# Kernel optimization log

Measured on AMD Instinct MI355X. Metric: run time of the kernel, lower is better.

The kernel has to match this reference:

```python
import jax, jax.numpy as jnp
import numpy as np

B, N, H, D, DEPTH = 16, 1024, 2, 128, 3
A = H * D  # atten_dim = 256
FFN = 1024
EPS = 1e-5


def layer_norm(x, g, b):
    mu = jnp.mean(x, axis=-1, keepdims=True)
    var = jnp.mean(jnp.square(x - mu), axis=-1, keepdims=True)
    return (x - mu) * jax.lax.rsqrt(var + EPS) * g + b


def setup_inputs() -> dict:
    key = jax.random.key(0)
    ks = jax.random.split(key, 16)
    s = lambda fan_in: 1.0 / np.sqrt(fan_in)
    inp = {
        "X": jax.random.normal(ks[0], (B, N, A), jnp.float32),
        # per-layer attention projections, stacked over depth
        "Wq": jax.random.normal(ks[1], (DEPTH, A, A), jnp.float32) * s(A),
        "bq": jnp.zeros((DEPTH, A), jnp.float32),
        "Wk": jax.random.normal(ks[2], (DEPTH, A, A), jnp.float32) * s(A),
        "bk": jnp.zeros((DEPTH, A), jnp.float32),
        "Wv": jax.random.normal(ks[3], (DEPTH, A, A), jnp.float32) * s(A),
        "bv": jnp.zeros((DEPTH, A), jnp.float32),
        # per-layer FFN (roll_out): Linear(A,1024)+ReLU, Linear(1024,A)+ReLU
        "W1": jax.random.normal(ks[4], (DEPTH, A, FFN), jnp.float32) * s(A),
        "b1": jnp.zeros((DEPTH, FFN), jnp.float32),
        "W2": jax.random.normal(ks[5], (DEPTH, FFN, A), jnp.float32) * s(FFN),
        "b2": jnp.zeros((DEPTH, A), jnp.float32),
        # single shared LayerNorm (the torch module reuses one instance)
        "ln_g": jnp.ones((A,), jnp.float32),
        "ln_b": jnp.zeros((A,), jnp.float32),
        # Conv1d(A, A, kernel_size=1) == per-position linear over channels
        "Wc": jax.random.normal(ks[6], (A, A), jnp.float32) * s(A),
        "bc": jnp.zeros((A,), jnp.float32),
        # final Linear(A, A) on pooled features
        "We": jax.random.normal(ks[7], (A, A), jnp.float32) * s(A),
        "be": jnp.zeros((A,), jnp.float32),
    }
    return inp


def reference(X, Wq, bq, Wk, bk, Wv, bv, W1, b1, W2, b2, ln_g, ln_b, Wc, bc, We, be):
    inv_sqrt_d = 1.0 / np.sqrt(D)
    step = X  # [B, N, A]
    for i in range(DEPTH):
        q = (step @ Wq[i] + bq[i]).reshape(B, N, H, D).transpose(0, 2, 1, 3)
        k = (step @ Wk[i] + bk[i]).reshape(B, N, H, D).transpose(0, 2, 1, 3)
        v = (step @ Wv[i] + bv[i]).reshape(B, N, H, D).transpose(0, 2, 1, 3)
        scores = jnp.einsum('bhqd,bhkd->bhqk', q, k) * inv_sqrt_d
        probs = jax.nn.softmax(scores, axis=-1)
        attn = jnp.einsum('bhqk,bhkd->bhqd', probs, v)
        attn = attn.transpose(0, 2, 1, 3).reshape(B, N, A)
        roll = jax.nn.relu(jax.nn.relu(attn @ W1[i] + b1[i]) @ W2[i] + b2[i])
        step = layer_norm(roll + step, ln_g, ln_b)
    # Conv1d(kernel=1) + ReLU over channels, per position
    entity_encodings = jax.nn.relu(step @ Wc + bc)  # [B, N, A]
    pooled = jnp.mean(entity_encodings, axis=1)      # [B, A]
    encoded_entities = jax.nn.relu(pooled @ We + be)  # [B, A]
    return encoded_entities
```

## Files before the change

kernel.cpp:

```cpp
#include <hip/hip_runtime.h>
#include <hip/hip_bf16.h>
#include <cstddef>

#define B_   16
#define N_   1024
#define H_   2
#define D_   128
#define A_   256
#define FFN_ 1024
#define M_   (B_ * N_)
#define EPS_ 1e-5f
#define SPLIT 4
#define KT   32
#define TPC  (N_ / SPLIT / KT)
#define QKV_E ((size_t)B_ * H_ * N_ * D_)

typedef short  short8  __attribute__((ext_vector_type(8)));
typedef float  f32x16  __attribute__((ext_vector_type(16)));
typedef unsigned int uint;
typedef unsigned short ushort;

#define MFMA32(a, b, c) __builtin_amdgcn_mfma_f32_32x32x16_bf16(a, b, c, 0, 0, 0)

__device__ __forceinline__ uint f2b1(float x) {
    uint u = __float_as_uint(x);
    return (u + 0x7fffu + ((u >> 16) & 1u)) >> 16;
}
__device__ __forceinline__ uint f2b2(float lo, float hi) {
    return f2b1(lo) | (f2b1(hi) << 16);
}
__device__ __forceinline__ float b2f(ushort u) {
    return __uint_as_float(((uint)u) << 16);
}

__global__ __launch_bounds__(256) void f32_to_bf16_kernel(
    const float* __restrict__ in, ushort* __restrict__ out)
{
    const size_t i = ((size_t)blockIdx.x * 256 + threadIdx.x) * 8;
    float4 a = *(const float4*)(in + i);
    float4 b = *(const float4*)(in + i + 4);
    uint4 w = { f2b2(a.x, a.y), f2b2(a.z, a.w), f2b2(b.x, b.y), f2b2(b.z, b.w) };
    *(uint4*)(out + i) = w;
}

__global__ __launch_bounds__(256) void prep_kernel(
    const float* __restrict__ Wq, const float* __restrict__ Wk,
    const float* __restrict__ Wv, const float* __restrict__ W1,
    const float* __restrict__ W2, const float* __restrict__ Wc,
    ushort* __restrict__ wqkv_t, ushort* __restrict__ w1_t,
    ushort* __restrict__ w2_t, ushort* __restrict__ wc_t)
{
    const int z = blockIdx.z;
    const float* W; ushort* out; int K, N, n0, k0;
    if (z < 9) {
        const int layer = z / 3, sec = z % 3;
        W = (sec == 0 ? Wq : sec == 1 ? Wk : Wv) + (size_t)layer * A_ * A_;
        out = wqkv_t + (size_t)layer * 3 * A_ * A_ + (size_t)sec * A_ * A_;
        K = A_; N = A_;
        n0 = blockIdx.x * 32; k0 = blockIdx.y * 32;
    } else if (z < 12) {
        const int layer = z - 9;
        W = W1 + (size_t)layer * A_ * FFN_; out = w1_t + (size_t)layer * A_ * FFN_;
        K = A_; N = FFN_;
        n0 = blockIdx.x * 32; k0 = blockIdx.y * 32;
    } else if (z < 15) {
        const int layer = z - 12;
        W = W2 + (size_t)layer * FFN_ * A_; out = w2_t + (size_t)layer * FFN_ * A_;
        K = FFN_; N = A_;
        k0 = blockIdx.x * 32; n0 = blockIdx.y * 32;
    } else {
        W = Wc; out = wc_t; K = A_; N = A_;
        n0 = blockIdx.x * 32; k0 = blockIdx.y * 32;
    }
    if (n0 >= N || k0 >= K) return;

    __shared__ float tile[32][33];
    const int tc = threadIdx.x & 31, tr = threadIdx.x >> 5;
#pragma unroll
    for (int it = 0; it < 4; ++it) {
        int r = it * 8 + tr;
        tile[r][tc] = W[(size_t)(k0 + r) * N + n0 + tc];
    }
    __syncthreads();
#pragma unroll
    for (int it = 0; it < 4; ++it) {
        int r = it * 8 + tr;
        out[(size_t)(n0 + r) * K + k0 + tc] = (ushort)f2b1(tile[tc][r]);
    }
}

template <int MR>
__global__ __launch_bounds__(256) void gemm_mfma(
    const ushort* __restrict__ Asrc, const ushort* __restrict__ Wt,
    const float* __restrict__ bias, const float* __restrict__ biasK,
    const float* __restrict__ biasV, void* __restrict__ outp,
    int K, int ldc, int mode)
{
    constexpr int BM = MR * 64;
    __shared__ ushort sA[BM * 72];
    __shared__ ushort sB[128 * 72];

    const int tid = threadIdx.x;
    const int wid = tid >> 6, lane = tid & 63;
    const int c = lane & 31, g = lane >> 5;
    const int wr = wid >> 1, wc = wid & 1;
    const int m0 = blockIdx.x * BM;
    const int n0 = blockIdx.y * 128;

    f32x16 acc[MR][2] = {};

    for (int k0 = 0; k0 < K; k0 += 64) {
        __syncthreads();
#pragma unroll
        for (int it = 0; it < BM / 32; ++it) {
            int idx = it * 256 + tid, r = idx >> 3, cc = (idx & 7) * 8;
            *(uint4*)&sA[r * 72 + cc] =
                *(const uint4*)(Asrc + (size_t)(m0 + r) * K + k0 + cc);
        }
#pragma unroll
        for (int it = 0; it < 4; ++it) {
            int idx = it * 256 + tid, r = idx >> 3, cc = (idx & 7) * 8;
            *(uint4*)&sB[r * 72 + cc] =
                *(const uint4*)(Wt + (size_t)(n0 + r) * K + k0 + cc);
        }
        __syncthreads();
#pragma unroll
        for (int ks = 0; ks < 4; ++ks) {
            const int ko = ks * 16 + 8 * g;
            short8 b0 = *(const short8*)&sB[(wc * 64 + c) * 72 + ko];
            short8 b1 = *(const short8*)&sB[(wc * 64 + 32 + c) * 72 + ko];
#pragma unroll
            for (int mr = 0; mr < MR; ++mr) {
                short8 a = *(const short8*)&sA[((wr * MR + mr) * 32 + c) * 72 + ko];
                acc[mr][0] = MFMA32(a, b0, acc[mr][0]);
                acc[mr][1] = MFMA32(a, b1, acc[mr][1]);
            }
        }
    }

    const int sec = n0 >> 8;
    const float* bp = bias;
    int nw = n0;
    if (mode == 5) {
        bp = (sec == 0 ? bias : sec == 1 ? biasK : biasV);
        nw = n0 & 255;
    }
    const float bz[2] = { bp[nw + wc * 64 + c], bp[nw + wc * 64 + 32 + c] };

    float colsum[2] = { 0.f, 0.f };

#pragma unroll
    for (int mr = 0; mr < MR; ++mr) {
#pragma unroll
        for (int ct = 0; ct < 2; ++ct) {
            const int colbase = n0 + wc * 64 + ct * 32 + c;
#pragma unroll
            for (int rg = 0; rg < 4; ++rg) {
                const int row = m0 + (wr * MR + mr) * 32 + 8 * rg + 4 * g;
                float v0 = acc[mr][ct][4 * rg + 0] + bz[ct];
                float v1 = acc[mr][ct][4 * rg + 1] + bz[ct];
                float v2 = acc[mr][ct][4 * rg + 2] + bz[ct];
                float v3 = acc[mr][ct][4 * rg + 3] + bz[ct];
                if (mode == 1 || mode == 2 || mode == 6) {
                    v0 = fmaxf(v0, 0.f); v1 = fmaxf(v1, 0.f);
                    v2 = fmaxf(v2, 0.f); v3 = fmaxf(v3, 0.f);
                }
                if (mode == 1) {
                    float* o = (float*)outp;
                    o[(size_t)(row + 0) * ldc + colbase] = v0;
                    o[(size_t)(row + 1) * ldc + colbase] = v1;
                    o[(size_t)(row + 2) * ldc + colbase] = v2;
                    o[(size_t)(row + 3) * ldc + colbase] = v3;
                } else if (mode == 2) {
                    ushort* o = (ushort*)outp;
                    o[(size_t)(row + 0) * ldc + colbase] = (ushort)f2b1(v0);
                    o[(size_t)(row + 1) * ldc + colbase] = (ushort)f2b1(v1);
                    o[(size_t)(row + 2) * ldc + colbase] = (ushort)f2b1(v2);
                    o[(size_t)(row + 3) * ldc + colbase] = (ushort)f2b1(v3);
                } else if (mode == 6) {
                    colsum[ct] += v0 + v1 + v2 + v3;
                } else {
                    const int cw = colbase & 255;
                    const int hh = cw >> 7, dd = cw & (D_ - 1);
                    if (sec < 2) {
                        ushort* o = (ushort*)outp + (size_t)sec * QKV_E;
#pragma unroll
                        for (int r2 = 0; r2 < 4; ++r2) {
                            int rw = row + r2;
                            int bb = rw >> 10, np = rw & (N_ - 1);
                            float vv = (r2 == 0 ? v0 : r2 == 1 ? v1 : r2 == 2 ? v2 : v3);
                            size_t off = (((size_t)(bb * H_ + hh) * 32 + (np >> 5)) * 16
                                          + (dd >> 3)) * 256
                                         + (np & 31) * 8 + (dd & 7);
                            o[off] = (ushort)f2b1(vv);
                        }
                    } else {
                        ushort* o = (ushort*)outp + 2 * QKV_E;
                        const int bb = row >> 10, np = row & (N_ - 1);
                        size_t off = ((((size_t)(bb * H_ + hh) * 32 + (np >> 5)) * 4
                                       + (dd >> 5)) * 4 + ((np & 31) >> 3)) * 256
                                     + (dd & 31) * 8 + (np & 7);
                        uint2 w = { f2b2(v0, v1), f2b2(v2, v3) };
                        *(uint2*)(o + off) = w;
                    }
                }
            }
        }
    }

    if (mode == 6) {
        float* part = (float*)outp;
        const int b = m0 >> 10;
#pragma unroll
        for (int ct = 0; ct < 2; ++ct) {
            float cs = colsum[ct] + __shfl_xor(colsum[ct], 32, 64);
            if (g == 0)
                atomicAdd(&part[(size_t)b * A_ + n0 + wc * 64 + ct * 32 + c], cs);
        }
    }
}

#define OPITCH 132

__global__ __launch_bounds__(128, 3) void attn_kernel(
    const ushort* __restrict__ qg, const ushort* __restrict__ kg,
    const ushort* __restrict__ vtg, ushort* __restrict__ po,
    float* __restrict__ pm, float* __restrict__ pl)
{
    __shared__ ushort sO[64 * OPITCH];

    const int tid = threadIdx.x;
    const int w = tid >> 6, lane = tid & 63;
    const int c = lane & 31, g = lane >> 5;

    const int flat = blockIdx.x;
    const int xcd  = flat & 7;
    const int ii   = flat >> 3;
    const int pair = xcd * 16 + (ii & 15);
    const int qt   = ii >> 4;
    const int bh   = pair & 31;
    const int z    = pair >> 5;

    const int q0 = qt * 64 + w * 32;
    const float scale2 = 0.08838834764831845f * 1.44269504f;
    const float THR = 11.5f;
    const int lo8 = c * 8;

    short8 qf[8];
    const ushort* qt_ = qg + ((size_t)bh * 32 + (q0 >> 5)) * 4096;
#pragma unroll
    for (int ks = 0; ks < 8; ++ks)
        qf[ks] = *(const short8*)(qt_ + (2 * ks + g) * 256 + lo8);

    f32x16 oacc[4] = {};
    float m = -1e30f, l = 0.f;

    for (int t = 0; t < TPC; ++t) {
        const size_t tb = ((size_t)bh * 32 + z * 8 + t) * 4096;
        const ushort* kt_ = kg + tb;
        const ushort* vt_ = vtg + tb;

        f32x16 sacc = {};
        __builtin_amdgcn_s_setprio(1);
#pragma unroll
        for (int ks = 0; ks < 8; ++ks) {
            short8 a = *(const short8*)(kt_ + (2 * ks + g) * 256 + lo8);
            sacc = MFMA32(a, qf[ks], sacc);
        }
        __builtin_amdgcn_s_setprio(0);

        const ushort* vb = vt_ + g * 256 + lo8;
        short8 vfA0 = *(const short8*)(vb + 0 * 1024);
        short8 vfA1 = *(const short8*)(vb + 1 * 1024);
        short8 vfA2 = *(const short8*)(vb + 2 * 1024);
        short8 vfA3 = *(const short8*)(vb + 3 * 1024);
        short8 vfB0 = *(const short8*)(vb + 0 * 1024 + 512);
        short8 vfB1 = *(const short8*)(vb + 1 * 1024 + 512);
        short8 vfB2 = *(const short8*)(vb + 2 * 1024 + 512);
        short8 vfB3 = *(const short8*)(vb + 3 * 1024 + 512);
        __builtin_amdgcn_sched_barrier(0);

        float p[16];
        float tmax = -1e30f;
#pragma unroll
        for (int r = 0; r < 16; ++r) {
            float s = sacc[r] * scale2;
            p[r] = s;
            tmax = fmaxf(tmax, s);
        }
        tmax = fmaxf(tmax, __shfl_xor(tmax, 32, 64));
        if (!__all(tmax - m <= THR)) {
            const float mnew = fmaxf(m, tmax);
            const float corr = exp2f(m - mnew);
#pragma unroll
            for (int dt = 0; dt < 4; ++dt)
#pragma unroll
                for (int r = 0; r < 16; ++r) oacc[dt][r] *= corr;
            l *= corr;
            m = mnew;
        }
        float tsum = 0.f;
#pragma unroll
        for (int r = 0; r < 16; ++r) {
            p[r] = exp2f(p[r] - m);
            tsum += p[r];
        }
        tsum += __shfl_xor(tsum, 32, 64);
        l += tsum;

        uint pk[8];
#pragma unroll
        for (int pp = 0; pp < 8; ++pp)
            pk[pp] = f2b2(p[2 * pp], p[2 * pp + 1]);

        uint v0 = g ? pk[0] : pk[2];
        uint v1 = g ? pk[1] : pk[3];
        uint v2 = g ? pk[4] : pk[6];
        uint v3 = g ? pk[5] : pk[7];
        uint r0 = (uint)__shfl_xor((int)v0, 32, 64);
        uint r1 = (uint)__shfl_xor((int)v1, 32, 64);
        uint r2 = (uint)__shfl_xor((int)v2, 32, 64);
        uint r3 = (uint)__shfl_xor((int)v3, 32, 64);

        __builtin_amdgcn_s_setprio(1);
#pragma unroll
        for (int kb = 0; kb < 2; ++kb) {
            union { uint u[4]; short8 s; } pf;
            if (kb == 0) {
                pf.u[0] = g ? r0 : pk[0];
                pf.u[1] = g ? r1 : pk[1];
                pf.u[2] = g ? pk[2] : r0;
                pf.u[3] = g ? pk[3] : r1;
            } else {
                pf.u[0] = g ? r2 : pk[4];
                pf.u[1] = g ? r3 : pk[5];
                pf.u[2] = g ? pk[6] : r2;
                pf.u[3] = g ? pk[7] : r3;
            }
            oacc[0] = MFMA32(kb ? vfB0 : vfA0, pf.s, oacc[0]);
            oacc[1] = MFMA32(kb ? vfB1 : vfA1, pf.s, oacc[1]);
            oacc[2] = MFMA32(kb ? vfB2 : vfA2, pf.s, oacc[2]);
            oacc[3] = MFMA32(kb ? vfB3 : vfA3, pf.s, oacc[3]);
        }
        __builtin_amdgcn_s_setprio(0);
    }

    if (lane < 32) {
        pm[(size_t)(z * 32 + bh) * N_ + q0 + c] = m;
        pl[(size_t)(z * 32 + bh) * N_ + q0 + c] = l;
    }
    {
        const int qrl = w * 32 + c;
#pragma unroll
        for (int dt = 0; dt < 4; ++dt)
#pragma unroll
            for (int rg = 0; rg < 4; ++rg) {
                int d = dt * 32 + 8 * rg + 4 * g;
                uint2 pv = { f2b2(oacc[dt][4 * rg + 0], oacc[dt][4 * rg + 1]),
                             f2b2(oacc[dt][4 * rg + 2], oacc[dt][4 * rg + 3]) };
                *(uint2*)&sO[qrl * OPITCH + d] = pv;
            }
    }
    __syncthreads();
    {
        const size_t pbase = ((size_t)(z * 32 + bh) * N_ + qt * 64) * D_;
#pragma unroll
        for (int it = 0; it < 16; ++it) {
            int idx = it * 128 + tid;
            int r = idx >> 5, dgr = (idx & 31) * 4;
            uint2 v = *(const uint2*)&sO[r * OPITCH + dgr];
            *(uint2*)(po + pbase + (size_t)r * D_ + dgr) = v;
        }
    }
}

__global__ __launch_bounds__(256) void combine_kernel(
    const ushort* __restrict__ po, const float* __restrict__ pm,
    const float* __restrict__ pl, ushort* __restrict__ out)
{
    const int idx = blockIdx.x * 256 + threadIdx.x;
    const int row = idx >> 4, d0 = (idx & 15) * 8;
    const int R = B_ * H_ * N_;

    float ms[SPLIT];
    float M = -1e30f;
#pragma unroll
    for (int s = 0; s < SPLIT; ++s) {
        ms[s] = pm[(size_t)s * R + row];
        M = fmaxf(M, ms[s]);
    }
    float L = 0.f;
    float acc[8] = {};
#pragma unroll
    for (int s = 0; s < SPLIT; ++s) {
        float wgt = exp2f(ms[s] - M);
        L += pl[(size_t)s * R + row] * wgt;
        uint4 pv = *(const uint4*)(po + ((size_t)s * R + row) * D_ + d0);
        const ushort* pu = (const ushort*)&pv;
#pragma unroll
        for (int j = 0; j < 8; ++j) acc[j] += b2f(pu[j]) * wgt;
    }
    const float inv = 1.f / L;
    uint4 w;
    w.x = f2b2(acc[0] * inv, acc[1] * inv);
    w.y = f2b2(acc[2] * inv, acc[3] * inv);
    w.z = f2b2(acc[4] * inv, acc[5] * inv);
    w.w = f2b2(acc[6] * inv, acc[7] * inv);
    const int bh = row >> 10, n = row & (N_ - 1);
    const int bb = bh >> 1, hh = bh & 1;
    *(uint4*)(out + ((size_t)(bb * N_ + n)) * A_ + hh * D_ + d0) = w;
}

__global__ __launch_bounds__(256) void add_ln_kernel(
    const ushort* __restrict__ roll, const float* __restrict__ prev,
    const float* __restrict__ g, const float* __restrict__ bta,
    float* __restrict__ out, ushort* __restrict__ outb)
{
    const int row = blockIdx.x * 4 + (threadIdx.x >> 6);
    const int lane = threadIdx.x & 63, c4 = lane * 4;
    const size_t base = (size_t)row * A_ + c4;

    uint2 rb = *(const uint2*)(roll + base);
    float4 pv = *(const float4*)(prev + base);
    float v0 = b2f((ushort)(rb.x & 0xffff)) + pv.x;
    float v1 = b2f((ushort)(rb.x >> 16))    + pv.y;
    float v2 = b2f((ushort)(rb.y & 0xffff)) + pv.z;
    float v3 = b2f((ushort)(rb.y >> 16))    + pv.w;

    float s  = v0 + v1 + v2 + v3;
    float s2 = v0 * v0 + v1 * v1 + v2 * v2 + v3 * v3;
#pragma unroll
    for (int o = 32; o > 0; o >>= 1) {
        s  += __shfl_xor(s, o, 64);
        s2 += __shfl_xor(s2, o, 64);
    }
    const float mu = s * (1.f / A_);
    const float rs = rsqrtf(s2 * (1.f / A_) - mu * mu + EPS_);

    float4 gv = *(const float4*)(g + c4);
    float4 bv = *(const float4*)(bta + c4);
    float y0 = (v0 - mu) * rs * gv.x + bv.x;
    float y1 = (v1 - mu) * rs * gv.y + bv.y;
    float y2 = (v2 - mu) * rs * gv.z + bv.z;
    float y3 = (v3 - mu) * rs * gv.w + bv.w;

    float4 yo = { y0, y1, y2, y3 };
    *(float4*)(out + base) = yo;
    uint2 yb = { f2b2(y0, y1), f2b2(y2, y3) };
    *(uint2*)(outb + base) = yb;
}

__global__ __launch_bounds__(256) void final_kernel(
    const float* __restrict__ part, const float* __restrict__ We,
    const float* __restrict__ be, float* __restrict__ out)
{
    __shared__ float sp[A_];
    const int b = blockIdx.x, tid = threadIdx.x;
    sp[tid] = part[(size_t)b * A_ + tid] * (1.0f / N_);
    __syncthreads();
    float acc = be[tid];
    for (int kk = 0; kk < A_; ++kk) acc += sp[kk] * We[(size_t)kk * A_ + tid];
    out[b * A_ + tid] = fmaxf(acc, 0.f);
}

extern "C" void kernel_launch(void* const* d_in, const int* in_sizes, int n_in,
                              void* d_out, int out_size, void* d_ws, size_t ws_size,
                              hipStream_t stream)
{
    const float* X    = (const float*)d_in[0];
    const float* Wq   = (const float*)d_in[1];
    const float* bq   = (const float*)d_in[2];
    const float* Wk   = (const float*)d_in[3];
    const float* bk   = (const float*)d_in[4];
    const float* Wv   = (const float*)d_in[5];
    const float* bv   = (const float*)d_in[6];
    const float* W1   = (const float*)d_in[7];
    const float* b1   = (const float*)d_in[8];
    const float* W2   = (const float*)d_in[9];
    const float* b2   = (const float*)d_in[10];
    const float* ln_g = (const float*)d_in[11];
    const float* ln_b = (const float*)d_in[12];
    const float* Wc   = (const float*)d_in[13];
    const float* bc   = (const float*)d_in[14];
    const float* We   = (const float*)d_in[15];
    const float* be   = (const float*)d_in[16];

    char* base = (char*)d_ws;
    ushort* qb     = (ushort*)base;  base += QKV_E * 2;
                             base += QKV_E * 2;
                             base += QKV_E * 2;
    ushort* hbuf   = (ushort*)base;  base += (size_t)M_ * FFN_ * 2;
    ushort* rollb  = (ushort*)base;  base += (size_t)M_ * A_ * 2;
    float*  step   = (float*)base;   base += (size_t)M_ * A_ * 4;
    ushort* stepb  = (ushort*)base;  base += (size_t)M_ * A_ * 2;
    ushort* wqkv_t = (ushort*)base;  base += (size_t)3 * 3 * A_ * A_ * 2;
    ushort* w1_t   = (ushort*)base;  base += (size_t)3 * A_ * FFN_ * 2;
    ushort* w2_t   = (ushort*)base;  base += (size_t)3 * FFN_ * A_ * 2;
    ushort* wc_t   = (ushort*)base;  base += (size_t)A_ * A_ * 2;
    float*  part   = (float*)base;   base += (size_t)B_ * A_ * 4;
    float*  pm     = (float*)base;   base += (size_t)SPLIT * B_ * H_ * N_ * 4;
    float*  pl     = (float*)base;   base += (size_t)SPLIT * B_ * H_ * N_ * 4;
    ushort* kbuf   = qb + QKV_E;
    ushort* vtbuf  = qb + 2 * QKV_E;
    ushort* po     = hbuf;
    ushort* attnb  = qb;

    prep_kernel<<<dim3(32, 8, 16), 256, 0, stream>>>(
        Wq, Wk, Wv, W1, W2, Wc, wqkv_t, w1_t, w2_t, wc_t);
    f32_to_bf16_kernel<<<(M_ * A_) / (256 * 8), 256, 0, stream>>>(X, stepb);

    const float* cur = X;
    for (int i = 0; i < 3; ++i) {
        gemm_mfma<2><<<dim3(M_/128, 6), 256, 0, stream>>>(
            stepb, wqkv_t + (size_t)i * 3 * A_ * A_,
            bq + i * A_, bk + i * A_, bv + i * A_, qb, A_, 0, 5);

        attn_kernel<<<16 * SPLIT * B_ * H_, 128, 0, stream>>>(
            qb, kbuf, vtbuf, po, pm, pl);
        combine_kernel<<<(B_*H_*N_*D_)/(256*8), 256, 0, stream>>>(po, pm, pl, attnb);

        gemm_mfma<2><<<dim3(M_/128, FFN_/128), 256, 0, stream>>>(
            attnb, w1_t + (size_t)i * A_ * FFN_, b1 + i * FFN_, nullptr, nullptr,
            hbuf, A_, FFN_, 2);
        gemm_mfma<1><<<dim3(M_/64, A_/128), 256, 0, stream>>>(
            hbuf, w2_t + (size_t)i * FFN_ * A_, b2 + i * A_, nullptr, nullptr,
            rollb, FFN_, A_, 2);

        add_ln_kernel<<<M_/4, 256, 0, stream>>>(rollb, cur, ln_g, ln_b, step, stepb);
        cur = step;
    }

    hipMemsetAsync(part, 0, (size_t)B_ * A_ * 4, stream);
    gemm_mfma<1><<<dim3(M_/64, A_/128), 256, 0, stream>>>(
        stepb, wc_t, bc, nullptr, nullptr, part, A_, 0, 6);
    final_kernel<<<B_, 256, 0, stream>>>(part, We, be, (float*)d_out);
}
```

Measured before the change: 385.1 us.

## Prefetch next K tile in attention and keep residual stream in bf16

The attention kernel now loads the next K tile into registers while the current tile's QK MFMAs run, and issues the V loads before the score MFMAs. Launch bounds are lowered from 3 to 2 blocks per SM to make room for the extra registers. The add+LayerNorm kernel no longer reads and writes a float32 residual. It reads the bf16 step buffer as the residual and updates it in place, which cuts memory traffic but lowers the precision of the residual path, including the first layer's use of X.

```diff
diff --git a/kernel.cpp b/kernel.cpp
--- a/kernel.cpp
+++ b/kernel.cpp
@@ -222,7 +222,7 @@
 
 #define OPITCH 132
 
-__global__ __launch_bounds__(128, 3) void attn_kernel(
+__global__ __launch_bounds__(128, 2) void attn_kernel(
     const ushort* __restrict__ qg, const ushort* __restrict__ kg,
     const ushort* __restrict__ vtg, ushort* __restrict__ po,
     float* __restrict__ pm, float* __restrict__ pl)
@@ -255,21 +255,21 @@
     f32x16 oacc[4] = {};
     float m = -1e30f, l = 0.f;
 
+    const size_t chunk0 = ((size_t)bh * 32 + z * 8) * 4096;
+    const ushort* kb0 = kg + chunk0 + g * 256 + lo8;
+    short8 kf0 = *(const short8*)(kb0 + 0 * 512);
+    short8 kf1 = *(const short8*)(kb0 + 1 * 512);
+    short8 kf2 = *(const short8*)(kb0 + 2 * 512);
+    short8 kf3 = *(const short8*)(kb0 + 3 * 512);
+    short8 kf4 = *(const short8*)(kb0 + 4 * 512);
+    short8 kf5 = *(const short8*)(kb0 + 5 * 512);
+    short8 kf6 = *(const short8*)(kb0 + 6 * 512);
+    short8 kf7 = *(const short8*)(kb0 + 7 * 512);
+
     for (int t = 0; t < TPC; ++t) {
-        const size_t tb = ((size_t)bh * 32 + z * 8 + t) * 4096;
-        const ushort* kt_ = kg + tb;
-        const ushort* vt_ = vtg + tb;
-
-        f32x16 sacc = {};
-        __builtin_amdgcn_s_setprio(1);
-#pragma unroll
-        for (int ks = 0; ks < 8; ++ks) {
-            short8 a = *(const short8*)(kt_ + (2 * ks + g) * 256 + lo8);
-            sacc = MFMA32(a, qf[ks], sacc);
-        }
-        __builtin_amdgcn_s_setprio(0);
-
-        const ushort* vb = vt_ + g * 256 + lo8;
+        const size_t tb = chunk0 + (size_t)t * 4096;
+
+        const ushort* vb = vtg + tb + g * 256 + lo8;
         short8 vfA0 = *(const short8*)(vb + 0 * 1024);
         short8 vfA1 = *(const short8*)(vb + 1 * 1024);
         short8 vfA2 = *(const short8*)(vb + 2 * 1024);
@@ -278,6 +278,31 @@
         short8 vfB1 = *(const short8*)(vb + 1 * 1024 + 512);
         short8 vfB2 = *(const short8*)(vb + 2 * 1024 + 512);
         short8 vfB3 = *(const short8*)(vb + 3 * 1024 + 512);
+        __builtin_amdgcn_sched_barrier(0);
+
+        f32x16 sacc = {};
+        __builtin_amdgcn_s_setprio(1);
+        sacc = MFMA32(kf0, qf[0], sacc);
+        sacc = MFMA32(kf1, qf[1], sacc);
+        sacc = MFMA32(kf2, qf[2], sacc);
+        sacc = MFMA32(kf3, qf[3], sacc);
+        sacc = MFMA32(kf4, qf[4], sacc);
+        sacc = MFMA32(kf5, qf[5], sacc);
+        sacc = MFMA32(kf6, qf[6], sacc);
+        sacc = MFMA32(kf7, qf[7], sacc);
+        __builtin_amdgcn_s_setprio(0);
+
+        if (t + 1 < TPC) {
+            const ushort* kb2 = kg + tb + 4096 + g * 256 + lo8;
+            kf0 = *(const short8*)(kb2 + 0 * 512);
+            kf1 = *(const short8*)(kb2 + 1 * 512);
+            kf2 = *(const short8*)(kb2 + 2 * 512);
+            kf3 = *(const short8*)(kb2 + 3 * 512);
+            kf4 = *(const short8*)(kb2 + 4 * 512);
+            kf5 = *(const short8*)(kb2 + 5 * 512);
+            kf6 = *(const short8*)(kb2 + 6 * 512);
+            kf7 = *(const short8*)(kb2 + 7 * 512);
+        }
         __builtin_amdgcn_sched_barrier(0);
 
         float p[16];
@@ -412,20 +437,19 @@
 }
 
 __global__ __launch_bounds__(256) void add_ln_kernel(
-    const ushort* __restrict__ roll, const float* __restrict__ prev,
-    const float* __restrict__ g, const float* __restrict__ bta,
-    float* __restrict__ out, ushort* __restrict__ outb)
+    const ushort* __restrict__ roll, ushort* __restrict__ stepb,
+    const float* __restrict__ g, const float* __restrict__ bta)
 {
     const int row = blockIdx.x * 4 + (threadIdx.x >> 6);
     const int lane = threadIdx.x & 63, c4 = lane * 4;
     const size_t base = (size_t)row * A_ + c4;
 
     uint2 rb = *(const uint2*)(roll + base);
-    float4 pv = *(const float4*)(prev + base);
-    float v0 = b2f((ushort)(rb.x & 0xffff)) + pv.x;
-    float v1 = b2f((ushort)(rb.x >> 16))    + pv.y;
-    float v2 = b2f((ushort)(rb.y & 0xffff)) + pv.z;
-    float v3 = b2f((ushort)(rb.y >> 16))    + pv.w;
+    uint2 pb = *(const uint2*)(stepb + base);
+    float v0 = b2f((ushort)(rb.x & 0xffff)) + b2f((ushort)(pb.x & 0xffff));
+    float v1 = b2f((ushort)(rb.x >> 16))    + b2f((ushort)(pb.x >> 16));
+    float v2 = b2f((ushort)(rb.y & 0xffff)) + b2f((ushort)(pb.y & 0xffff));
+    float v3 = b2f((ushort)(rb.y >> 16))    + b2f((ushort)(pb.y >> 16));
 
     float s  = v0 + v1 + v2 + v3;
     float s2 = v0 * v0 + v1 * v1 + v2 * v2 + v3 * v3;
@@ -444,10 +468,8 @@
     float y2 = (v2 - mu) * rs * gv.z + bv.z;
     float y3 = (v3 - mu) * rs * gv.w + bv.w;
 
-    float4 yo = { y0, y1, y2, y3 };
-    *(float4*)(out + base) = yo;
     uint2 yb = { f2b2(y0, y1), f2b2(y2, y3) };
-    *(uint2*)(outb + base) = yb;
+    *(uint2*)(stepb + base) = yb;
 }
 
 __global__ __launch_bounds__(256) void final_kernel(
@@ -491,7 +513,6 @@
                              base += QKV_E * 2;
     ushort* hbuf   = (ushort*)base;  base += (size_t)M_ * FFN_ * 2;
     ushort* rollb  = (ushort*)base;  base += (size_t)M_ * A_ * 2;
-    float*  step   = (float*)base;   base += (size_t)M_ * A_ * 4;
     ushort* stepb  = (ushort*)base;  base += (size_t)M_ * A_ * 2;
     ushort* wqkv_t = (ushort*)base;  base += (size_t)3 * 3 * A_ * A_ * 2;
     ushort* w1_t   = (ushort*)base;  base += (size_t)3 * A_ * FFN_ * 2;
@@ -509,7 +530,6 @@
         Wq, Wk, Wv, W1, W2, Wc, wqkv_t, w1_t, w2_t, wc_t);
     f32_to_bf16_kernel<<<(M_ * A_) / (256 * 8), 256, 0, stream>>>(X, stepb);
 
-    const float* cur = X;
     for (int i = 0; i < 3; ++i) {
         gemm_mfma<2><<<dim3(M_/128, 6), 256, 0, stream>>>(
             stepb, wqkv_t + (size_t)i * 3 * A_ * A_,
@@ -526,8 +546,7 @@
             hbuf, w2_t + (size_t)i * FFN_ * A_, b2 + i * A_, nullptr, nullptr,
             rollb, FFN_, A_, 2);
 
-        add_ln_kernel<<<M_/4, 256, 0, stream>>>(rollb, cur, ln_g, ln_b, step, stepb);
-        cur = step;
+        add_ln_kernel<<<M_/4, 256, 0, stream>>>(rollb, stepb, ln_g, ln_b);
     }
 
     hipMemsetAsync(part, 0, (size_t)B_ * A_ * 4, stream);
```

Result: faster. 365.6 us (-5.1%).
